# Kernel optimization log

Hardware: AMD Instinct MI355X
Metric: run time of the kernel (lower is better)

## Reference

```python
import jax, jax.numpy as jnp
import numpy as np

B, H, O, E, CMAP = 8192, 1024, 256, 16, 1000


def setup_inputs() -> dict:
    key = jax.random.key(0)
    k_x, k_w, k_b, k_num, k_c = jax.random.split(key, 5)
    x = jax.random.normal(k_x, (B, H), dtype=jnp.float32)
    num = jax.random.randint(k_num, (B,), 0, CMAP, dtype=jnp.int64)
    c = jax.random.randint(k_c, (CMAP,), 0, E, dtype=jnp.int64)
    # per-expert Linear params (torch default: uniform(-1/sqrt(H), 1/sqrt(H)))
    bound = 1.0 / np.sqrt(H)
    W = jax.random.uniform(k_w, (E, O, H), dtype=jnp.float32, minval=-bound, maxval=bound)
    b = jax.random.uniform(k_b, (E, O), dtype=jnp.float32, minval=-bound, maxval=bound)
    return {"x": x, "W": W, "b": b, "num": num, "c": c}


def reference(x, W, b, num, c):
    # expert id for each sample: layers[c[num[i]]]
    expert = c[num]  # [B]
    # compute all experts' linear outputs in one batched GEMM, then select.
    # logits: [B, E, O]
    logits = jnp.einsum('bh,eoh->beo', x, W) + b[None, :, :]
    sel = jnp.take_along_axis(logits, expert[:, None, None], axis=1)[:, 0, :]  # [B, O]
    return jax.nn.sigmoid(sel)
```

## Files before the change

### kernel.cpp

```cpp
#include <hip/hip_runtime.h>
#include <hip/hip_bf16.h>
#include <stdint.h>

#define B_N   8192
#define H_K   1024
#define O_N   256
#define E_N   16
#define RCAP  1024

#define TILE_M    32
#define TILE_N    128
#define BK        64
#define NITER     (H_K / BK)
#define MTILES    (RCAP / TILE_M)
#define LDS_LD    (BK + 8)

#define WS_CURSOR   0
#define WS_ROWBUF   1024
#define WS_WBF16    131072

typedef __attribute__((ext_vector_type(8))) short  short8;
typedef __attribute__((ext_vector_type(4))) float  float4v;

__device__ __forceinline__ short f32_to_bf16(float f) {
    uint32_t u = __builtin_bit_cast(uint32_t, f);
    u += 0x7fffu + ((u >> 16) & 1u);
    return (short)(u >> 16);
}

__device__ __forceinline__ short8 cvt8(float4v v0, float4v v1) {
    short8 s;
    s[0] = f32_to_bf16(v0[0]); s[1] = f32_to_bf16(v0[1]);
    s[2] = f32_to_bf16(v0[2]); s[3] = f32_to_bf16(v0[3]);
    s[4] = f32_to_bf16(v1[0]); s[5] = f32_to_bf16(v1[1]);
    s[6] = f32_to_bf16(v1[2]); s[7] = f32_to_bf16(v1[3]);
    return s;
}

__device__ __forceinline__ float4v mfma16(short8 a, short8 b, float4v c) {
    return __builtin_amdgcn_mfma_f32_16x16x32_bf16(a, b, c, 0, 0, 0);
}

__device__ __forceinline__ void gl2lds16(const void* gsrc, void* ldst) {
    __builtin_amdgcn_global_load_lds(
        (const __attribute__((address_space(1))) uint32_t*)gsrc,
        (__attribute__((address_space(3))) uint32_t*)ldst, 16, 0, 0);
}

__global__ __launch_bounds__(256) void
k_prep(const float* __restrict__ W, const int* __restrict__ num, const int* __restrict__ c,
       int* __restrict__ cursor, int* __restrict__ rowbuf, short* __restrict__ Wb) {
    const int tid = threadIdx.x;
    const int bx  = blockIdx.x;

    if (bx < E_N) {
        unsigned mask = 0;
#pragma unroll
        for (int u = 0; u < 32; ++u) {
            const int i = u * 256 + tid;
            const int e = c[num[i]];
            mask |= (unsigned)(e == bx) << u;
        }
        const int cnt = __popc(mask);
        const int lane = tid & 63, wv = tid >> 6;
        int incl = cnt;
#pragma unroll
        for (int d = 1; d < 64; d <<= 1) {
            int v = __shfl_up(incl, d, 64);
            if (lane >= d) incl += v;
        }
        __shared__ int wsum[4];
        if (lane == 63) wsum[wv] = incl;
        __syncthreads();
        int base = 0;
        for (int w = 0; w < wv; ++w) base += wsum[w];
        int pos = base + incl - cnt;
        for (int u = 0; u < 32; ++u)
            if ((mask >> u) & 1u) rowbuf[bx * RCAP + pos++] = u * 256 + tid;
        if (tid == 255) cursor[bx] = base + incl;
    }

    const int nchunk = E_N * O_N * H_K / 8;
    const int stride = 256 * 256;
    for (int ch = bx * 256 + tid; ch < nchunk; ch += stride) {
        const float4v* src = (const float4v*)(W + (size_t)ch * 8);
        *(short8*)(Wb + (size_t)ch * 8) = cvt8(src[0], src[1]);
    }
}

__global__ __launch_bounds__(256) void
k_gemm(const float* __restrict__ x, const short* __restrict__ Wb,
       const float* __restrict__ bias, const int* __restrict__ cursor,
       const int* __restrict__ rowbuf, float* __restrict__ out) {
    const int e = blockIdx.x;
    int count = cursor[e]; if (count > RCAP) count = RCAP;
    const int m0 = blockIdx.y * TILE_M;
    if (m0 >= count) return;
    const int n0 = blockIdx.z * TILE_N;

    __shared__ short xs[2][TILE_M][LDS_LD];
    __shared__ short wsh[2][TILE_N][BK];
    __shared__ int   rows[TILE_M];

    const int tid = threadIdx.x;
    if (tid < TILE_M)
        rows[tid] = (m0 + tid < count) ? rowbuf[e * RCAP + m0 + tid] : -1;
    __syncthreads();

    const int r8   = tid >> 3;
    const int scol = (tid & 7) * 8;
    const int xrow = rows[r8];

    const int lane = tid & 63;
    const int wave = tid >> 6;
    const int wm = wave >> 1, wn = wave & 1;
    const int quad = lane >> 4, l16 = lane & 15;

    const int sub = lane >> 3;
    const int clx = (lane & 7) ^ sub;

    const short* wseg = Wb + (size_t)(e * O_N + n0) * H_K;

    float4v xv0, xv1;
    auto load_x = [&](int k0) {
        if (xrow >= 0) {
            const float4v* p = (const float4v*)(x + (size_t)xrow * H_K + k0 + scol);
            xv0 = p[0]; xv1 = p[1];
        } else { xv0 = (float4v)0.0f; xv1 = (float4v)0.0f; }
    };
    auto store_x = [&](int buf) {
        *(short8*)&xs[buf][r8][scol] = cvt8(xv0, xv1);
    };
    auto issue_w = [&](int buf, int k0) {
#pragma unroll
        for (int u = 0; u < 4; ++u) {
            const int q = wave * 4 + u;
            gl2lds16(wseg + (size_t)(q * 8 + sub) * H_K + k0 + clx * 8,
                     &wsh[buf][q * 8][0]);
        }
    };

    float4v acc[4];
#pragma unroll
    for (int j = 0; j < 4; ++j) acc[j] = (float4v)0.0f;

    load_x(0);
    issue_w(0, 0);
    store_x(0);

    for (int k = 0; k < NITER; ++k) {
        const int cur = k & 1;
        __syncthreads();
        if (k + 1 < NITER) {
            load_x((k + 1) * BK);
            issue_w(1 - cur, (k + 1) * BK);
        }

#pragma unroll
        for (int ks = 0; ks < 2; ++ks) {
            const int kx = ks * 32 + quad * 8;
            const int cw = (((ks * 4 + quad) ^ (l16 & 7))) * 8;
            short8 a  = *(const short8*)&xs[cur][wm * 16 + l16][kx];
            short8 b0 = *(const short8*)&wsh[cur][wn * 64 + l16][cw];
            short8 b1 = *(const short8*)&wsh[cur][wn * 64 + 16 + l16][cw];
            short8 b2 = *(const short8*)&wsh[cur][wn * 64 + 32 + l16][cw];
            short8 b3 = *(const short8*)&wsh[cur][wn * 64 + 48 + l16][cw];
            acc[0] = mfma16(a, b0, acc[0]);
            acc[1] = mfma16(a, b1, acc[1]);
            acc[2] = mfma16(a, b2, acc[2]);
            acc[3] = mfma16(a, b3, acc[3]);
        }

        if (k + 1 < NITER) store_x(1 - cur);
    }

#pragma unroll
    for (int j = 0; j < 4; ++j) {
        const int colg = n0 + wn * 64 + j * 16 + l16;
        const float bv = bias[e * O_N + colg];
        const int rl = wm * 16 + quad * 4;
#pragma unroll
        for (int reg = 0; reg < 4; ++reg) {
            const int rid = rows[rl + reg];
            if (rid >= 0) {
                const float v = acc[j][reg] + bv;
                out[(size_t)rid * O_N + colg] = 1.0f / (1.0f + __expf(-v));
            }
        }
    }
}

extern "C" void kernel_launch(void* const* d_in, const int* in_sizes, int n_in,
                              void* d_out, int out_size, void* d_ws, size_t ws_size,
                              hipStream_t stream) {
    const float* x   = (const float*)d_in[0];
    const float* W   = (const float*)d_in[1];
    const float* b   = (const float*)d_in[2];
    const int*   num = (const int*)d_in[3];
    const int*   c   = (const int*)d_in[4];
    float* out = (float*)d_out;

    char*  ws     = (char*)d_ws;
    int*   cursor = (int*)(ws + WS_CURSOR);
    int*   rowbuf = (int*)(ws + WS_ROWBUF);
    short* Wb     = (short*)(ws + WS_WBF16);

    k_prep<<<256, 256, 0, stream>>>(W, num, c, cursor, rowbuf, Wb);

    dim3 gg(E_N, MTILES, O_N / TILE_N);
    k_gemm<<<gg, 256, 0, stream>>>(x, Wb, b, cursor, rowbuf, out);
}
```

Baseline: 115.9 us.

## Pre-convert x to bf16 and use LDS-free single-wave register-pipelined GEMM

The prep kernel now converts x to bf16 as well as W, using blocks 16-255 so the routing blocks return early. The GEMM drops shared memory and barriers. Each 64-thread wave loads its A and B fragments straight from global memory into registers, double-buffered, and computes a 32x64 tile. This removes LDS traffic, the syncs and the per-tile x conversion, at the cost of an extra full pass over x in prep, lost reuse across waves, and more global and L2 loads.

```diff
diff --git a/kernel.cpp b/kernel.cpp
--- a/kernel.cpp
+++ b/kernel.cpp
@@ -8,16 +8,13 @@
 #define E_N   16
 #define RCAP  1024
 
-#define TILE_M    32
-#define TILE_N    128
-#define BK        64
-#define NITER     (H_K / BK)
-#define MTILES    (RCAP / TILE_M)
-#define LDS_LD    (BK + 8)
+#define BK    64
+#define NITER (H_K / BK)
 
 #define WS_CURSOR   0
 #define WS_ROWBUF   1024
 #define WS_WBF16    131072
+#define WS_XBF16    (131072 + 8388608)
 
 typedef __attribute__((ext_vector_type(8))) short  short8;
 typedef __attribute__((ext_vector_type(4))) float  float4v;
@@ -41,15 +38,11 @@
     return __builtin_amdgcn_mfma_f32_16x16x32_bf16(a, b, c, 0, 0, 0);
 }
 
-__device__ __forceinline__ void gl2lds16(const void* gsrc, void* ldst) {
-    __builtin_amdgcn_global_load_lds(
-        (const __attribute__((address_space(1))) uint32_t*)gsrc,
-        (__attribute__((address_space(3))) uint32_t*)ldst, 16, 0, 0);
-}
-
 __global__ __launch_bounds__(256) void
-k_prep(const float* __restrict__ W, const int* __restrict__ num, const int* __restrict__ c,
-       int* __restrict__ cursor, int* __restrict__ rowbuf, short* __restrict__ Wb) {
+k_prep(const float* __restrict__ W, const float* __restrict__ x,
+       const int* __restrict__ num, const int* __restrict__ c,
+       int* __restrict__ cursor, int* __restrict__ rowbuf,
+       short* __restrict__ Wb, short* __restrict__ xb) {
     const int tid = threadIdx.x;
     const int bx  = blockIdx.x;
 
@@ -78,113 +71,103 @@
         for (int u = 0; u < 32; ++u)
             if ((mask >> u) & 1u) rowbuf[bx * RCAP + pos++] = u * 256 + tid;
         if (tid == 255) cursor[bx] = base + incl;
+        return;
     }
 
-    const int nchunk = E_N * O_N * H_K / 8;
-    const int stride = 256 * 256;
-    for (int ch = bx * 256 + tid; ch < nchunk; ch += stride) {
+    const int stride = 240 * 256;
+    const int t0 = (bx - 16) * 256 + tid;
+    const int NW = E_N * O_N * H_K / 8;
+    for (int ch = t0; ch < NW; ch += stride) {
         const float4v* src = (const float4v*)(W + (size_t)ch * 8);
         *(short8*)(Wb + (size_t)ch * 8) = cvt8(src[0], src[1]);
     }
+    const int NX = B_N * H_K / 8;
+    for (int ch = t0; ch < NX; ch += stride) {
+        const float4v* src = (const float4v*)(x + (size_t)ch * 8);
+        *(short8*)(xb + (size_t)ch * 8) = cvt8(src[0], src[1]);
+    }
 }
 
-__global__ __launch_bounds__(256) void
-k_gemm(const float* __restrict__ x, const short* __restrict__ Wb,
+__global__ __launch_bounds__(64) void
+k_gemm(const short* __restrict__ xb, const short* __restrict__ Wb,
        const float* __restrict__ bias, const int* __restrict__ cursor,
        const int* __restrict__ rowbuf, float* __restrict__ out) {
     const int e = blockIdx.x;
     int count = cursor[e]; if (count > RCAP) count = RCAP;
-    const int m0 = blockIdx.y * TILE_M;
+    const int m0 = blockIdx.y * 32;
     if (m0 >= count) return;
-    const int n0 = blockIdx.z * TILE_N;
+    const int n0 = blockIdx.z * 64;
 
-    __shared__ short xs[2][TILE_M][LDS_LD];
-    __shared__ short wsh[2][TILE_N][BK];
-    __shared__ int   rows[TILE_M];
-
-    const int tid = threadIdx.x;
-    if (tid < TILE_M)
-        rows[tid] = (m0 + tid < count) ? rowbuf[e * RCAP + m0 + tid] : -1;
-    __syncthreads();
-
-    const int r8   = tid >> 3;
-    const int scol = (tid & 7) * 8;
-    const int xrow = rows[r8];
-
-    const int lane = tid & 63;
-    const int wave = tid >> 6;
-    const int wm = wave >> 1, wn = wave & 1;
+    const int lane = threadIdx.x;
     const int quad = lane >> 4, l16 = lane & 15;
 
-    const int sub = lane >> 3;
-    const int clx = (lane & 7) ^ sub;
+    int ra[2];
+#pragma unroll
+    for (int mb = 0; mb < 2; ++mb) {
+        const int pos = m0 + mb * 16 + l16;
+        ra[mb] = (pos < count) ? rowbuf[e * RCAP + pos] : 0;
+    }
 
-    const short* wseg = Wb + (size_t)(e * O_N + n0) * H_K;
+    const short* ap0 = xb + (size_t)ra[0] * H_K + quad * 8;
+    const short* ap1 = xb + (size_t)ra[1] * H_K + quad * 8;
+    const short* bp0 = Wb + (size_t)(e * O_N + n0 +  0 + l16) * H_K + quad * 8;
+    const short* bp1 = Wb + (size_t)(e * O_N + n0 + 16 + l16) * H_K + quad * 8;
+    const short* bp2 = Wb + (size_t)(e * O_N + n0 + 32 + l16) * H_K + quad * 8;
+    const short* bp3 = Wb + (size_t)(e * O_N + n0 + 48 + l16) * H_K + quad * 8;
 
-    float4v xv0, xv1;
-    auto load_x = [&](int k0) {
-        if (xrow >= 0) {
-            const float4v* p = (const float4v*)(x + (size_t)xrow * H_K + k0 + scol);
-            xv0 = p[0]; xv1 = p[1];
-        } else { xv0 = (float4v)0.0f; xv1 = (float4v)0.0f; }
-    };
-    auto store_x = [&](int buf) {
-        *(short8*)&xs[buf][r8][scol] = cvt8(xv0, xv1);
-    };
-    auto issue_w = [&](int buf, int k0) {
+    float4v acc[2][4];
 #pragma unroll
-        for (int u = 0; u < 4; ++u) {
-            const int q = wave * 4 + u;
-            gl2lds16(wseg + (size_t)(q * 8 + sub) * H_K + k0 + clx * 8,
-                     &wsh[buf][q * 8][0]);
+    for (int i = 0; i < 2; ++i)
+#pragma unroll
+        for (int j = 0; j < 4; ++j) acc[i][j] = (float4v)0.0f;
+
+    struct Set { short8 a[2][2]; short8 b[2][4]; };
+    Set s0, s1;
+
+    auto load = [&](Set& s, int k0) {
+#pragma unroll
+        for (int ks = 0; ks < 2; ++ks) {
+            const int off = k0 + ks * 32;
+            s.a[ks][0] = *(const short8*)(ap0 + off);
+            s.a[ks][1] = *(const short8*)(ap1 + off);
+            s.b[ks][0] = *(const short8*)(bp0 + off);
+            s.b[ks][1] = *(const short8*)(bp1 + off);
+            s.b[ks][2] = *(const short8*)(bp2 + off);
+            s.b[ks][3] = *(const short8*)(bp3 + off);
         }
     };
+    auto comp = [&](Set& s) {
+#pragma unroll
+        for (int ks = 0; ks < 2; ++ks)
+#pragma unroll
+            for (int mb = 0; mb < 2; ++mb)
+#pragma unroll
+                for (int nb = 0; nb < 4; ++nb)
+                    acc[mb][nb] = mfma16(s.a[ks][mb], s.b[ks][nb], acc[mb][nb]);
+    };
 
-    float4v acc[4];
+    load(s0, 0);
 #pragma unroll
-    for (int j = 0; j < 4; ++j) acc[j] = (float4v)0.0f;
-
-    load_x(0);
-    issue_w(0, 0);
-    store_x(0);
-
-    for (int k = 0; k < NITER; ++k) {
-        const int cur = k & 1;
-        __syncthreads();
-        if (k + 1 < NITER) {
-            load_x((k + 1) * BK);
-            issue_w(1 - cur, (k + 1) * BK);
-        }
-
-#pragma unroll
-        for (int ks = 0; ks < 2; ++ks) {
-            const int kx = ks * 32 + quad * 8;
-            const int cw = (((ks * 4 + quad) ^ (l16 & 7))) * 8;
-            short8 a  = *(const short8*)&xs[cur][wm * 16 + l16][kx];
-            short8 b0 = *(const short8*)&wsh[cur][wn * 64 + l16][cw];
-            short8 b1 = *(const short8*)&wsh[cur][wn * 64 + 16 + l16][cw];
-            short8 b2 = *(const short8*)&wsh[cur][wn * 64 + 32 + l16][cw];
-            short8 b3 = *(const short8*)&wsh[cur][wn * 64 + 48 + l16][cw];
-            acc[0] = mfma16(a, b0, acc[0]);
-            acc[1] = mfma16(a, b1, acc[1]);
-            acc[2] = mfma16(a, b2, acc[2]);
-            acc[3] = mfma16(a, b3, acc[3]);
-        }
-
-        if (k + 1 < NITER) store_x(1 - cur);
+    for (int k = 0; k < NITER; k += 2) {
+        if (k + 1 < NITER) load(s1, (k + 1) * BK);
+        comp(s0);
+        if (k + 2 < NITER) load(s0, (k + 2) * BK);
+        comp(s1);
     }
 
 #pragma unroll
-    for (int j = 0; j < 4; ++j) {
-        const int colg = n0 + wn * 64 + j * 16 + l16;
-        const float bv = bias[e * O_N + colg];
-        const int rl = wm * 16 + quad * 4;
+    for (int mb = 0; mb < 2; ++mb) {
 #pragma unroll
         for (int reg = 0; reg < 4; ++reg) {
-            const int rid = rows[rl + reg];
-            if (rid >= 0) {
-                const float v = acc[j][reg] + bv;
-                out[(size_t)rid * O_N + colg] = 1.0f / (1.0f + __expf(-v));
+            const int pos = m0 + mb * 16 + quad * 4 + reg;
+            if (pos < count) {
+                const int rid = rowbuf[e * RCAP + pos];
+#pragma unroll
+                for (int nb = 0; nb < 4; ++nb) {
+                    const int col = n0 + nb * 16 + l16;
+                    const float v = acc[mb][nb][reg] + bias[e * O_N + col];
+                    out[(size_t)rid * O_N + col] = 1.0f / (1.0f + __expf(-v));
+                }
             }
         }
     }
@@ -204,9 +187,10 @@
     int*   cursor = (int*)(ws + WS_CURSOR);
     int*   rowbuf = (int*)(ws + WS_ROWBUF);
     short* Wb     = (short*)(ws + WS_WBF16);
+    short* xb     = (short*)(ws + WS_XBF16);
 
-    k_prep<<<256, 256, 0, stream>>>(W, num, c, cursor, rowbuf, Wb);
+    k_prep<<<256, 256, 0, stream>>>(W, x, num, c, cursor, rowbuf, Wb, xb);
 
-    dim3 gg(E_N, MTILES, O_N / TILE_N);
-    k_gemm<<<gg, 256, 0, stream>>>(x, Wb, b, cursor, rowbuf, out);
+    dim3 gg(E_N, RCAP / 32, O_N / 64);
+    k_gemm<<<gg, 64, 0, stream>>>(xb, Wb, b, cursor, rowbuf, out);
 }
```

After: 146.1 us. +26.0%, slower.
